# Kernel optimization log

Measured on AMD Instinct MI355X. Metric: run time of the kernel, lower is better.

The kernel has to match this reference:

```python
import jax, jax.numpy as jnp
import numpy as np

EPS = 1e-10

def _quantize_one(x, codebook):
    # x: [B, T, D]; codebook: [K, D]
    B, T, D = x.shape
    K = codebook.shape[0]
    flat = x.reshape(-1, D)  # [N, D]
    # squared euclidean distance (argmin of this == argmax of -dist in torch code)
    dist = (jnp.sum(flat * flat, axis=-1, keepdims=True)
            - 2.0 * flat @ codebook.T
            + jnp.sum(codebook * codebook, axis=-1))  # [N, K]
    ind = jnp.argmin(dist, axis=-1)  # [N]
    q = codebook[ind].reshape(B, T, D)
    # commitment loss: mse(quantize.detach(), x) * commitment(=1.0)
    loss = jnp.mean((jax.lax.stop_gradient(q) - x) ** 2)
    # straight-through estimator
    q_st = x + jax.lax.stop_gradient(q - x)
    # perplexity from one-hot encodings
    counts = jnp.zeros((K,), dtype=x.dtype).at[ind].add(1.0)
    avg_probs = counts / ind.shape[0]
    perplexity = jnp.exp(-jnp.sum(avg_probs * jnp.log(avg_probs + EPS)))
    return q_st, loss, perplexity

def setup_inputs() -> dict:
    key = jax.random.key(0)
    k1, k2 = jax.random.split(key)
    z = jax.random.normal(k1, (16, 64, 4096), dtype=jnp.float32)
    codebooks = jax.random.normal(k2, (8, 1024, 64), dtype=jnp.float32)
    return {"z": z, "codebooks": codebooks}

def reference(z, codebooks):
    # z: [B, code_dim, T] -> transpose(2,1) -> [B, T, code_dim]
    x = jnp.transpose(z, (0, 2, 1))

    def step(carry, cb):
        residual, quantized_out = carry
        q, loss, perp = _quantize_one(residual, cb)
        return (residual - q, quantized_out + q), (loss, perp)

    (_, quantized_out), (losses, perplexities) = jax.lax.scan(
        step, (x, jnp.zeros_like(x)), codebooks)
    zq = jnp.transpose(quantized_out, (0, 2, 1))  # back to [B, code_dim, T]
    return zq, losses, perplexities
```

## Files before the change

kernel.cpp:

```cpp
#include <hip/hip_runtime.h>

#define S      8
#define K      1024
#define D      64
#define NVEC   65536
#define NW     2048
#define NELEM  4194304.0f
#define EPSQ   1e-10f
#define DELTA  0.005f

typedef __attribute__((ext_vector_type(8))) short  short8;
typedef __attribute__((ext_vector_type(4))) float  float4v;

static __device__ inline unsigned short f2bf(float f) {
    unsigned int u = __float_as_uint(f);
    u = (u + 0x7FFFu + ((u >> 16) & 1u)) >> 16;
    return (unsigned short)u;
}
static __device__ inline float bf2f(unsigned short h) {
    return __uint_as_float(((unsigned int)h) << 16);
}

__global__ void rvq_prep(const float* __restrict__ cb,
                         unsigned short* __restrict__ cbi,
                         float* __restrict__ c2, unsigned* __restrict__ cnt) {
    int i = blockIdx.x * blockDim.x + threadIdx.x;
    if (i < S * K) {
        const float* row = cb + (size_t)i * D;
        float a0 = 0.f, a1 = 0.f, a2 = 0.f, a3 = 0.f;
#pragma unroll
        for (int d = 0; d < D; d += 4) {
            a0 = fmaf(row[d+0], row[d+0], a0);
            a1 = fmaf(row[d+1], row[d+1], a1);
            a2 = fmaf(row[d+2], row[d+2], a2);
            a3 = fmaf(row[d+3], row[d+3], a3);
        }
        c2[i] = (a0 + a1) + (a2 + a3);
        cnt[i] = 0u;
    }
    int s  = i >> 12;
    int tau = (i >> 6) & 63;
    int l  = i & 63;
    int m  = l & 15, qq = l >> 4;
    const float* row = cb + (size_t)(s * K + tau * 16 + m) * D;
    short8 h0h, h0l, h1h, h1l;
#pragma unroll
    for (int e = 0; e < 8; ++e) {
        float x = row[qq * 8 + e];
        unsigned short h = f2bf(x);
        h0h[e] = (short)h; h0l[e] = (short)f2bf(x - bf2f(h));
        float y = row[32 + qq * 8 + e];
        unsigned short g = f2bf(y);
        h1h[e] = (short)g; h1l[e] = (short)f2bf(y - bf2f(g));
    }
    unsigned short* rec = cbi + (size_t)(s * 64 + tau) * 2048 + l * 8;
    *(short8*)(rec +    0) = h0h;
    *(short8*)(rec +  512) = h1h;
    *(short8*)(rec + 1024) = h0l;
    *(short8*)(rec + 1536) = h1l;
}

__global__ __launch_bounds__(64, 2)
void rvq_main(const float* __restrict__ z, const float* __restrict__ cbf,
              const unsigned short* __restrict__ cbi,
              const float* __restrict__ c2, float* __restrict__ zq,
              float* __restrict__ lossp, unsigned* __restrict__ cnt) {
    const int lane = threadIdx.x;
    const int m    = lane & 15;
    const int q    = lane >> 4;
    const int wid  = blockIdx.x;
    const int vbase = wid * 32;
    const int b    = vbase >> 12;
    const int ta   = (vbase & 4095) + m;
    const int tb   = ta + 16;
    const size_t zrow = ((size_t)(b * 64)) << 12;

    float ra0[8], ra1[8], rb0[8], rb1[8];
#pragma unroll
    for (int i = 0; i < 8; ++i) {
        ra0[i] = z[zrow + ((size_t)(q*8+i)    << 12) + ta];
        ra1[i] = z[zrow + ((size_t)(32+q*8+i) << 12) + ta];
        rb0[i] = z[zrow + ((size_t)(q*8+i)    << 12) + tb];
        rb1[i] = z[zrow + ((size_t)(32+q*8+i) << 12) + tb];
    }

#define LOADTILE(B0v, B1v, B2v, B3v, CCv, tt) {                              \
        const unsigned short* p_ = recs + (size_t)(tt) * 2048 + lane * 8;    \
        B0v = *(const short8*)(p_);                                          \
        B1v = *(const short8*)(p_ + 512);                                    \
        B2v = *(const short8*)(p_ + 1024);                                   \
        B3v = *(const short8*)(p_ + 1536);                                   \
        CCv = c2s[(tt) * 16 + m]; }

#pragma unroll 1
    for (int s = 0; s < S; ++s) {
        short8 xa0h, xa0l, xa1h, xa1l, xb0h, xb0l, xb1h, xb1l;
#pragma unroll
        for (int i = 0; i < 8; ++i) {
            unsigned short h;
            h = f2bf(ra0[i]); xa0h[i] = (short)h; xa0l[i] = (short)f2bf(ra0[i] - bf2f(h));
            h = f2bf(ra1[i]); xa1h[i] = (short)h; xa1l[i] = (short)f2bf(ra1[i] - bf2f(h));
            h = f2bf(rb0[i]); xb0h[i] = (short)h; xb0l[i] = (short)f2bf(rb0[i] - bf2f(h));
            h = f2bf(rb1[i]); xb1h[i] = (short)h; xb1l[i] = (short)f2bf(rb1[i] - bf2f(h));
        }

        float b1a[4], b2a[4], b1b[4], b2b[4];
        int   k1a[4], k1b[4];
#pragma unroll
        for (int j = 0; j < 4; ++j) {
            b1a[j] = 3.4e38f; b2a[j] = 3.4e38f; k1a[j] = 0;
            b1b[j] = 3.4e38f; b2b[j] = 3.4e38f; k1b[j] = 0;
        }

        const unsigned short* recs = cbi + (size_t)s * 131072;
        const float*          c2s  = c2 + s * K;

        short8 A0, A1, A2, A3, C0, C1, C2, C3;
        float  ca, cb2;
        LOADTILE(A0, A1, A2, A3, ca,  0);
        LOADTILE(C0, C1, C2, C3, cb2, 1);

#pragma unroll 1
        for (int tau = 0; tau < 64; tau += 2) {
            {
                short8 bh0 = A0, bh1 = A1, bl0 = A2, bl1 = A3;
                float  c2v = ca;
                if (tau + 2 < 64) LOADTILE(A0, A1, A2, A3, ca, tau + 2);
                float4v aa = {0.f,0.f,0.f,0.f}, ab = {0.f,0.f,0.f,0.f};
                aa = __builtin_amdgcn_mfma_f32_16x16x32_bf16(xa0h, bh0, aa, 0,0,0);
                aa = __builtin_amdgcn_mfma_f32_16x16x32_bf16(xa0l, bh0, aa, 0,0,0);
                aa = __builtin_amdgcn_mfma_f32_16x16x32_bf16(xa0h, bl0, aa, 0,0,0);
                aa = __builtin_amdgcn_mfma_f32_16x16x32_bf16(xa1h, bh1, aa, 0,0,0);
                aa = __builtin_amdgcn_mfma_f32_16x16x32_bf16(xa1l, bh1, aa, 0,0,0);
                aa = __builtin_amdgcn_mfma_f32_16x16x32_bf16(xa1h, bl1, aa, 0,0,0);
                ab = __builtin_amdgcn_mfma_f32_16x16x32_bf16(xb0h, bh0, ab, 0,0,0);
                ab = __builtin_amdgcn_mfma_f32_16x16x32_bf16(xb0l, bh0, ab, 0,0,0);
                ab = __builtin_amdgcn_mfma_f32_16x16x32_bf16(xb0h, bl0, ab, 0,0,0);
                ab = __builtin_amdgcn_mfma_f32_16x16x32_bf16(xb1h, bh1, ab, 0,0,0);
                ab = __builtin_amdgcn_mfma_f32_16x16x32_bf16(xb1l, bh1, ab, 0,0,0);
                ab = __builtin_amdgcn_mfma_f32_16x16x32_bf16(xb1h, bl1, ab, 0,0,0);
                int ncol = tau * 16 + m;
#pragma unroll
                for (int j = 0; j < 4; ++j) {
                    float sa = fmaf(-2.f, aa[j], c2v);
                    b2a[j] = fminf(b2a[j], fmaxf(sa, b1a[j]));
                    k1a[j] = (sa < b1a[j]) ? ncol : k1a[j];
                    b1a[j] = fminf(sa, b1a[j]);
                    float sb = fmaf(-2.f, ab[j], c2v);
                    b2b[j] = fminf(b2b[j], fmaxf(sb, b1b[j]));
                    k1b[j] = (sb < b1b[j]) ? ncol : k1b[j];
                    b1b[j] = fminf(sb, b1b[j]);
                }
            }
            {
                short8 bh0 = C0, bh1 = C1, bl0 = C2, bl1 = C3;
                float  c2v = cb2;
                if (tau + 3 < 64) LOADTILE(C0, C1, C2, C3, cb2, tau + 3);
                float4v aa = {0.f,0.f,0.f,0.f}, ab = {0.f,0.f,0.f,0.f};
                aa = __builtin_amdgcn_mfma_f32_16x16x32_bf16(xa0h, bh0, aa, 0,0,0);
                aa = __builtin_amdgcn_mfma_f32_16x16x32_bf16(xa0l, bh0, aa, 0,0,0);
                aa = __builtin_amdgcn_mfma_f32_16x16x32_bf16(xa0h, bl0, aa, 0,0,0);
                aa = __builtin_amdgcn_mfma_f32_16x16x32_bf16(xa1h, bh1, aa, 0,0,0);
                aa = __builtin_amdgcn_mfma_f32_16x16x32_bf16(xa1l, bh1, aa, 0,0,0);
                aa = __builtin_amdgcn_mfma_f32_16x16x32_bf16(xa1h, bl1, aa, 0,0,0);
                ab = __builtin_amdgcn_mfma_f32_16x16x32_bf16(xb0h, bh0, ab, 0,0,0);
                ab = __builtin_amdgcn_mfma_f32_16x16x32_bf16(xb0l, bh0, ab, 0,0,0);
                ab = __builtin_amdgcn_mfma_f32_16x16x32_bf16(xb0h, bl0, ab, 0,0,0);
                ab = __builtin_amdgcn_mfma_f32_16x16x32_bf16(xb1h, bh1, ab, 0,0,0);
                ab = __builtin_amdgcn_mfma_f32_16x16x32_bf16(xb1l, bh1, ab, 0,0,0);
                ab = __builtin_amdgcn_mfma_f32_16x16x32_bf16(xb1h, bl1, ab, 0,0,0);
                int ncol = (tau + 1) * 16 + m;
#pragma unroll
                for (int j = 0; j < 4; ++j) {
                    float sa = fmaf(-2.f, aa[j], c2v);
                    b2a[j] = fminf(b2a[j], fmaxf(sa, b1a[j]));
                    k1a[j] = (sa < b1a[j]) ? ncol : k1a[j];
                    b1a[j] = fminf(sa, b1a[j]);
                    float sb = fmaf(-2.f, ab[j], c2v);
                    b2b[j] = fminf(b2b[j], fmaxf(sb, b1b[j]));
                    k1b[j] = (sb < b1b[j]) ? ncol : k1b[j];
                    b1b[j] = fminf(sb, b1b[j]);
                }
            }
        }

#pragma unroll
        for (int off = 1; off < 16; off <<= 1) {
#pragma unroll
            for (int j = 0; j < 4; ++j) {
                float o1 = __shfl_xor(b1a[j], off); int ok = __shfl_xor(k1a[j], off);
                float o2 = __shfl_xor(b2a[j], off);
                float n2 = fminf(fminf(b2a[j], o2), fmaxf(b1a[j], o1));
                bool tk = (o1 < b1a[j]) || (o1 == b1a[j] && ok < k1a[j]);
                k1a[j] = tk ? ok : k1a[j]; b1a[j] = fminf(b1a[j], o1); b2a[j] = n2;
                o1 = __shfl_xor(b1b[j], off); ok = __shfl_xor(k1b[j], off);
                o2 = __shfl_xor(b2b[j], off);
                n2 = fminf(fminf(b2b[j], o2), fmaxf(b1b[j], o1));
                tk = (o1 < b1b[j]) || (o1 == b1b[j] && ok < k1b[j]);
                k1b[j] = tk ? ok : k1b[j]; b1b[j] = fminf(b1b[j], o1); b2b[j] = n2;
            }
        }

        const float* cr0 = cbf + (size_t)s * 65536;
#define RESCUE(b1X, b2X, k1X, R0, R1)                                         \
        for (int j = 0; j < 4; ++j) {                                         \
            unsigned long long mask = __ballot(b2X[j] - b1X[j] < DELTA);      \
            while (mask) {                                                    \
                int lq = (int)(__builtin_ctzll(mask)) >> 4;                   \
                mask &= ~(0xFFFFULL << (lq * 16));                            \
                int mrow = lq * 4 + j;                                        \
                float bd = 3.4e38f; int bk = 0;                               \
                for (int cc = 0; cc < 16; ++cc) {                             \
                    int n = cc * 64 + lane;                                   \
                    const float* crow = cr0 + (size_t)n * 64;                 \
                    float dot = 0.f;                                          \
                    for (int p = 0; p < 4; ++p) {                             \
                        for (int i = 0; i < 8; ++i)                           \
                            dot = fmaf(__shfl(R0[i], mrow + 16*p), crow[p*8+i], dot); \
                        for (int i = 0; i < 8; ++i)                           \
                            dot = fmaf(__shfl(R1[i], mrow + 16*p), crow[32+p*8+i], dot); \
                    }                                                         \
                    float sc = c2s[n] - 2.f * dot;                            \
                    if (sc < bd) { bd = sc; bk = n; }                         \
                }                                                             \
                for (int off = 1; off < 64; off <<= 1) {                      \
                    float ob = __shfl_xor(bd, off); int ok = __shfl_xor(bk, off); \
                    bool tk = (ob < bd) || (ob == bd && ok < bk);             \
                    bk = tk ? ok : bk; bd = fminf(bd, ob);                    \
                }                                                             \
                if (q == lq) k1X[j] = bk;                                     \
            }                                                                 \
        }
        RESCUE(b1a, b2a, k1a, ra0, ra1)
        RESCUE(b1b, b2b, k1b, rb0, rb1)
#undef RESCUE

        int mm = m & 3, src = (m >> 2) * 16;
        int wa0 = __shfl(k1a[0], src), wa1 = __shfl(k1a[1], src);
        int wa2 = __shfl(k1a[2], src), wa3 = __shfl(k1a[3], src);
        int bka = (mm == 0) ? wa0 : (mm == 1) ? wa1 : (mm == 2) ? wa2 : wa3;
        int wb0 = __shfl(k1b[0], src), wb1 = __shfl(k1b[1], src);
        int wb2 = __shfl(k1b[2], src), wb3 = __shfl(k1b[3], src);
        int bkb = (mm == 0) ? wb0 : (mm == 1) ? wb1 : (mm == 2) ? wb2 : wb3;

        const float* qa = cbf + (size_t)s * 65536 + (size_t)bka * 64;
        const float* qb = cbf + (size_t)s * 65536 + (size_t)bkb * 64;
#pragma unroll
        for (int i = 0; i < 8; ++i) {
            ra0[i] -= qa[q*8+i];  ra1[i] -= qa[32+q*8+i];
            rb0[i] -= qb[q*8+i];  rb1[i] -= qb[32+q*8+i];
        }

        float ls = 0.f;
#pragma unroll
        for (int i = 0; i < 8; ++i) {
            ls = fmaf(ra0[i], ra0[i], ls); ls = fmaf(ra1[i], ra1[i], ls);
            ls = fmaf(rb0[i], rb0[i], ls); ls = fmaf(rb1[i], rb1[i], ls);
        }
#pragma unroll
        for (int off = 1; off < 64; off <<= 1) ls += __shfl_xor(ls, off);
        if (lane == 0) lossp[s * NW + wid] = ls;

        if (q == 0) {
            atomicAdd(&cnt[s * K + bka], 1u);
            atomicAdd(&cnt[s * K + bkb], 1u);
        }
    }
#undef LOADTILE

#pragma unroll
    for (int i = 0; i < 8; ++i) {
        size_t a0 = zrow + ((size_t)(q*8+i)    << 12) + ta;
        size_t a1 = zrow + ((size_t)(32+q*8+i) << 12) + ta;
        zq[a0] = z[a0] - ra0[i];
        zq[a1] = z[a1] - ra1[i];
        size_t a2 = zrow + ((size_t)(q*8+i)    << 12) + tb;
        size_t a3 = zrow + ((size_t)(32+q*8+i) << 12) + tb;
        zq[a2] = z[a2] - rb0[i];
        zq[a3] = z[a3] - rb1[i];
    }
}

__global__ void rvq_finalize(const float* __restrict__ lossp,
                             const unsigned* __restrict__ cnt,
                             float* __restrict__ out_loss,
                             float* __restrict__ out_perp) {
    const int s   = blockIdx.x;
    const int tid = threadIdx.x;
    float ent = 0.f, lsum = 0.f;
    for (int i = tid; i < K; i += 256) {
        float p = (float)cnt[s * K + i] * (1.0f / 65536.0f);
        ent += p * logf(p + EPSQ);
    }
    for (int i = tid; i < NW; i += 256) lsum += lossp[s * NW + i];
    __shared__ float redE[4], redL[4];
#pragma unroll
    for (int off = 32; off > 0; off >>= 1) {
        ent  += __shfl_down(ent, off);
        lsum += __shfl_down(lsum, off);
    }
    if ((tid & 63) == 0) { redE[tid >> 6] = ent; redL[tid >> 6] = lsum; }
    __syncthreads();
    if (tid == 0) {
        float te = redE[0] + redE[1] + redE[2] + redE[3];
        float tl = redL[0] + redL[1] + redL[2] + redL[3];
        out_perp[s] = expf(-te);
        out_loss[s] = tl * (1.0f / NELEM);
    }
}

extern "C" void kernel_launch(void* const* d_in, const int* in_sizes, int n_in,
                              void* d_out, int out_size, void* d_ws, size_t ws_size,
                              hipStream_t stream) {
    const float* z  = (const float*)d_in[0];
    const float* cb = (const float*)d_in[1];

    float* zq       = (float*)d_out;
    float* out_loss = zq + 4194304;
    float* out_perp = out_loss + 8;

    char* ws = (char*)d_ws;
    unsigned short* cbi = (unsigned short*)(ws);
    float*    c2    = (float*)(ws + 2097152);
    unsigned* cnt   = (unsigned*)(ws + 2129920);
    float*    lossp = (float*)(ws + 2162688);

    hipLaunchKernelGGL(rvq_prep,     dim3(128),  dim3(256), 0, stream, cb, cbi, c2, cnt);
    hipLaunchKernelGGL(rvq_main,     dim3(NW),   dim3(64),  0, stream, z, cb, cbi, c2, zq, lossp, cnt);
    hipLaunchKernelGGL(rvq_finalize, dim3(S),    dim3(256), 0, stream, lossp, cnt, out_loss, out_perp);
}
```

Measured before the change: 465.8 us.

## Halve vectors per wave, fold -2 scale and c2 into MFMA accumulator

Each wave now handles 16 vectors instead of 32, doubling the grid to 4096 waves and raising launch bounds to 4 waves per SIMD, so more waves can hide latency. The codebook is pre-scaled by -2 in the prep kernel and the accumulator is seeded with c2, which removes the per-element FMA. The second-best update now uses fmed3, and the MFMA chain is wrapped in s_setprio. The trade-off is that each codebook tile loaded from memory is reused across half as many vectors, so codebook traffic per vector doubles. Scaling by -2 is exact, so the split-bf16 precision is unchanged.

Result: slower. 557.6 us (+19.7%).

```diff
diff --git a/kernel.cpp b/kernel.cpp
--- a/kernel.cpp
+++ b/kernel.cpp
@@ -4,7 +4,7 @@
 #define K      1024
 #define D      64
 #define NVEC   65536
-#define NW     2048
+#define NW     4096
 #define NELEM  4194304.0f
 #define EPSQ   1e-10f
 #define DELTA  0.005f
@@ -46,10 +46,10 @@
     short8 h0h, h0l, h1h, h1l;
 #pragma unroll
     for (int e = 0; e < 8; ++e) {
-        float x = row[qq * 8 + e];
+        float x = -2.0f * row[qq * 8 + e];
         unsigned short h = f2bf(x);
         h0h[e] = (short)h; h0l[e] = (short)f2bf(x - bf2f(h));
-        float y = row[32 + qq * 8 + e];
+        float y = -2.0f * row[32 + qq * 8 + e];
         unsigned short g = f2bf(y);
         h1h[e] = (short)g; h1l[e] = (short)f2bf(y - bf2f(g));
     }
@@ -60,7 +60,7 @@
     *(short8*)(rec + 1536) = h1l;
 }
 
-__global__ __launch_bounds__(64, 2)
+__global__ __launch_bounds__(64, 4)
 void rvq_main(const float* __restrict__ z, const float* __restrict__ cbf,
               const unsigned short* __restrict__ cbi,
               const float* __restrict__ c2, float* __restrict__ zq,
@@ -69,19 +69,16 @@
     const int m    = lane & 15;
     const int q    = lane >> 4;
     const int wid  = blockIdx.x;
-    const int vbase = wid * 32;
+    const int vbase = wid * 16;
     const int b    = vbase >> 12;
     const int ta   = (vbase & 4095) + m;
-    const int tb   = ta + 16;
     const size_t zrow = ((size_t)(b * 64)) << 12;
 
-    float ra0[8], ra1[8], rb0[8], rb1[8];
+    float ra0[8], ra1[8];
 #pragma unroll
     for (int i = 0; i < 8; ++i) {
         ra0[i] = z[zrow + ((size_t)(q*8+i)    << 12) + ta];
         ra1[i] = z[zrow + ((size_t)(32+q*8+i) << 12) + ta];
-        rb0[i] = z[zrow + ((size_t)(q*8+i)    << 12) + tb];
-        rb1[i] = z[zrow + ((size_t)(32+q*8+i) << 12) + tb];
     }
 
 #define LOADTILE(B0v, B1v, B2v, B3v, CCv, tt) {                              \
@@ -94,22 +91,19 @@
 
 #pragma unroll 1
     for (int s = 0; s < S; ++s) {
-        short8 xa0h, xa0l, xa1h, xa1l, xb0h, xb0l, xb1h, xb1l;
+        short8 xa0h, xa0l, xa1h, xa1l;
 #pragma unroll
         for (int i = 0; i < 8; ++i) {
             unsigned short h;
             h = f2bf(ra0[i]); xa0h[i] = (short)h; xa0l[i] = (short)f2bf(ra0[i] - bf2f(h));
             h = f2bf(ra1[i]); xa1h[i] = (short)h; xa1l[i] = (short)f2bf(ra1[i] - bf2f(h));
-            h = f2bf(rb0[i]); xb0h[i] = (short)h; xb0l[i] = (short)f2bf(rb0[i] - bf2f(h));
-            h = f2bf(rb1[i]); xb1h[i] = (short)h; xb1l[i] = (short)f2bf(rb1[i] - bf2f(h));
-        }
-
-        float b1a[4], b2a[4], b1b[4], b2b[4];
-        int   k1a[4], k1b[4];
+        }
+
+        float b1a[4], b2a[4];
+        int   k1a[4];
 #pragma unroll
         for (int j = 0; j < 4; ++j) {
             b1a[j] = 3.4e38f; b2a[j] = 3.4e38f; k1a[j] = 0;
-            b1b[j] = 3.4e38f; b2b[j] = 3.4e38f; k1b[j] = 0;
         }
 
         const unsigned short* recs = cbi + (size_t)s * 131072;
@@ -126,60 +120,44 @@
                 short8 bh0 = A0, bh1 = A1, bl0 = A2, bl1 = A3;
                 float  c2v = ca;
                 if (tau + 2 < 64) LOADTILE(A0, A1, A2, A3, ca, tau + 2);
-                float4v aa = {0.f,0.f,0.f,0.f}, ab = {0.f,0.f,0.f,0.f};
+                float4v aa = {c2v, c2v, c2v, c2v};
+                __builtin_amdgcn_s_setprio(1);
                 aa = __builtin_amdgcn_mfma_f32_16x16x32_bf16(xa0h, bh0, aa, 0,0,0);
                 aa = __builtin_amdgcn_mfma_f32_16x16x32_bf16(xa0l, bh0, aa, 0,0,0);
                 aa = __builtin_amdgcn_mfma_f32_16x16x32_bf16(xa0h, bl0, aa, 0,0,0);
                 aa = __builtin_amdgcn_mfma_f32_16x16x32_bf16(xa1h, bh1, aa, 0,0,0);
                 aa = __builtin_amdgcn_mfma_f32_16x16x32_bf16(xa1l, bh1, aa, 0,0,0);
                 aa = __builtin_amdgcn_mfma_f32_16x16x32_bf16(xa1h, bl1, aa, 0,0,0);
-                ab = __builtin_amdgcn_mfma_f32_16x16x32_bf16(xb0h, bh0, ab, 0,0,0);
-                ab = __builtin_amdgcn_mfma_f32_16x16x32_bf16(xb0l, bh0, ab, 0,0,0);
-                ab = __builtin_amdgcn_mfma_f32_16x16x32_bf16(xb0h, bl0, ab, 0,0,0);
-                ab = __builtin_amdgcn_mfma_f32_16x16x32_bf16(xb1h, bh1, ab, 0,0,0);
-                ab = __builtin_amdgcn_mfma_f32_16x16x32_bf16(xb1l, bh1, ab, 0,0,0);
-                ab = __builtin_amdgcn_mfma_f32_16x16x32_bf16(xb1h, bl1, ab, 0,0,0);
+                __builtin_amdgcn_s_setprio(0);
                 int ncol = tau * 16 + m;
 #pragma unroll
                 for (int j = 0; j < 4; ++j) {
-                    float sa = fmaf(-2.f, aa[j], c2v);
-                    b2a[j] = fminf(b2a[j], fmaxf(sa, b1a[j]));
+                    float sa = aa[j];
+                    b2a[j] = __builtin_amdgcn_fmed3f(sa, b1a[j], b2a[j]);
                     k1a[j] = (sa < b1a[j]) ? ncol : k1a[j];
                     b1a[j] = fminf(sa, b1a[j]);
-                    float sb = fmaf(-2.f, ab[j], c2v);
-                    b2b[j] = fminf(b2b[j], fmaxf(sb, b1b[j]));
-                    k1b[j] = (sb < b1b[j]) ? ncol : k1b[j];
-                    b1b[j] = fminf(sb, b1b[j]);
                 }
             }
             {
                 short8 bh0 = C0, bh1 = C1, bl0 = C2, bl1 = C3;
                 float  c2v = cb2;
                 if (tau + 3 < 64) LOADTILE(C0, C1, C2, C3, cb2, tau + 3);
-                float4v aa = {0.f,0.f,0.f,0.f}, ab = {0.f,0.f,0.f,0.f};
+                float4v aa = {c2v, c2v, c2v, c2v};
+                __builtin_amdgcn_s_setprio(1);
                 aa = __builtin_amdgcn_mfma_f32_16x16x32_bf16(xa0h, bh0, aa, 0,0,0);
                 aa = __builtin_amdgcn_mfma_f32_16x16x32_bf16(xa0l, bh0, aa, 0,0,0);
                 aa = __builtin_amdgcn_mfma_f32_16x16x32_bf16(xa0h, bl0, aa, 0,0,0);
                 aa = __builtin_amdgcn_mfma_f32_16x16x32_bf16(xa1h, bh1, aa, 0,0,0);
                 aa = __builtin_amdgcn_mfma_f32_16x16x32_bf16(xa1l, bh1, aa, 0,0,0);
                 aa = __builtin_amdgcn_mfma_f32_16x16x32_bf16(xa1h, bl1, aa, 0,0,0);
-                ab = __builtin_amdgcn_mfma_f32_16x16x32_bf16(xb0h, bh0, ab, 0,0,0);
-                ab = __builtin_amdgcn_mfma_f32_16x16x32_bf16(xb0l, bh0, ab, 0,0,0);
-                ab = __builtin_amdgcn_mfma_f32_16x16x32_bf16(xb0h, bl0, ab, 0,0,0);
-                ab = __builtin_amdgcn_mfma_f32_16x16x32_bf16(xb1h, bh1, ab, 0,0,0);
-                ab = __builtin_amdgcn_mfma_f32_16x16x32_bf16(xb1l, bh1, ab, 0,0,0);
-                ab = __builtin_amdgcn_mfma_f32_16x16x32_bf16(xb1h, bl1, ab, 0,0,0);
+                __builtin_amdgcn_s_setprio(0);
                 int ncol = (tau + 1) * 16 + m;
 #pragma unroll
                 for (int j = 0; j < 4; ++j) {
-                    float sa = fmaf(-2.f, aa[j], c2v);
-                    b2a[j] = fminf(b2a[j], fmaxf(sa, b1a[j]));
+                    float sa = aa[j];
+                    b2a[j] = __builtin_amdgcn_fmed3f(sa, b1a[j], b2a[j]);
                     k1a[j] = (sa < b1a[j]) ? ncol : k1a[j];
                     b1a[j] = fminf(sa, b1a[j]);
-                    float sb = fmaf(-2.f, ab[j], c2v);
-                    b2b[j] = fminf(b2b[j], fmaxf(sb, b1b[j]));
-                    k1b[j] = (sb < b1b[j]) ? ncol : k1b[j];
-                    b1b[j] = fminf(sb, b1b[j]);
                 }
             }
         }
@@ -193,11 +171,6 @@
                 float n2 = fminf(fminf(b2a[j], o2), fmaxf(b1a[j], o1));
                 bool tk = (o1 < b1a[j]) || (o1 == b1a[j] && ok < k1a[j]);
                 k1a[j] = tk ? ok : k1a[j]; b1a[j] = fminf(b1a[j], o1); b2a[j] = n2;
-                o1 = __shfl_xor(b1b[j], off); ok = __shfl_xor(k1b[j], off);
-                o2 = __shfl_xor(b2b[j], off);
-                n2 = fminf(fminf(b2b[j], o2), fmaxf(b1b[j], o1));
-                tk = (o1 < b1b[j]) || (o1 == b1b[j] && ok < k1b[j]);
-                k1b[j] = tk ? ok : k1b[j]; b1b[j] = fminf(b1b[j], o1); b2b[j] = n2;
             }
         }
 
@@ -232,39 +205,29 @@
             }                                                                 \
         }
         RESCUE(b1a, b2a, k1a, ra0, ra1)
-        RESCUE(b1b, b2b, k1b, rb0, rb1)
 #undef RESCUE
 
         int mm = m & 3, src = (m >> 2) * 16;
         int wa0 = __shfl(k1a[0], src), wa1 = __shfl(k1a[1], src);
         int wa2 = __shfl(k1a[2], src), wa3 = __shfl(k1a[3], src);
         int bka = (mm == 0) ? wa0 : (mm == 1) ? wa1 : (mm == 2) ? wa2 : wa3;
-        int wb0 = __shfl(k1b[0], src), wb1 = __shfl(k1b[1], src);
-        int wb2 = __shfl(k1b[2], src), wb3 = __shfl(k1b[3], src);
-        int bkb = (mm == 0) ? wb0 : (mm == 1) ? wb1 : (mm == 2) ? wb2 : wb3;
 
         const float* qa = cbf + (size_t)s * 65536 + (size_t)bka * 64;
-        const float* qb = cbf + (size_t)s * 65536 + (size_t)bkb * 64;
 #pragma unroll
         for (int i = 0; i < 8; ++i) {
             ra0[i] -= qa[q*8+i];  ra1[i] -= qa[32+q*8+i];
-            rb0[i] -= qb[q*8+i];  rb1[i] -= qb[32+q*8+i];
         }
 
         float ls = 0.f;
 #pragma unroll
         for (int i = 0; i < 8; ++i) {
             ls = fmaf(ra0[i], ra0[i], ls); ls = fmaf(ra1[i], ra1[i], ls);
-            ls = fmaf(rb0[i], rb0[i], ls); ls = fmaf(rb1[i], rb1[i], ls);
         }
 #pragma unroll
         for (int off = 1; off < 64; off <<= 1) ls += __shfl_xor(ls, off);
         if (lane == 0) lossp[s * NW + wid] = ls;
 
-        if (q == 0) {
-            atomicAdd(&cnt[s * K + bka], 1u);
-            atomicAdd(&cnt[s * K + bkb], 1u);
-        }
+        if (q == 0) atomicAdd(&cnt[s * K + bka], 1u);
     }
 #undef LOADTILE
 
@@ -274,10 +237,6 @@
         size_t a1 = zrow + ((size_t)(32+q*8+i) << 12) + ta;
         zq[a0] = z[a0] - ra0[i];
         zq[a1] = z[a1] - ra1[i];
-        size_t a2 = zrow + ((size_t)(q*8+i)    << 12) + tb;
-        size_t a3 = zrow + ((size_t)(32+q*8+i) << 12) + tb;
-        zq[a2] = z[a2] - rb0[i];
-        zq[a3] = z[a3] - rb1[i];
     }
 }
 
```
